# Kernel tuning notes

Hardware: AMD Instinct MI355X
Metric: run time of the kernel (lower is better)

Reference implementation:

```python
import jax, jax.numpy as jnp
import numpy as np

N, L, S, H, D = 2, 4096, 4096, 8, 64


def setup_inputs() -> dict:
    key = jax.random.key(0)
    kq, kk, kv = jax.random.split(key, 3)
    queries = jax.random.normal(kq, (N, L, H, D), dtype=jnp.float32)
    keys = jax.random.normal(kk, (N, S, H, D), dtype=jnp.float32)
    values = jax.random.normal(kv, (N, S, H, D), dtype=jnp.float32)
    return {"queries": queries, "keys": keys, "values": values}


def reference(queries, keys, values):
    # Full (non-fused) scaled dot-product attention, LoFTR FullAttention.
    # QK: [N, L, S, H]
    softmax_temp = 1.0 / jnp.sqrt(jnp.asarray(queries.shape[3], queries.dtype))
    QK = jnp.einsum('nlhd,nshd->nlsh', queries, keys)
    A = jax.nn.softmax(softmax_temp * QK, axis=2)  # softmax over S
    out = jnp.einsum('nlsh,nshd->nlhd', A, values)  # [N, L, H, D]
    return out
```

## Files before the change

kernel.cpp:

```cpp
#include <hip/hip_runtime.h>
#include <hip/hip_bf16.h>

typedef float  f32x4  __attribute__((ext_vector_type(4)));
typedef float  f32x16 __attribute__((ext_vector_type(16)));
typedef short  short8 __attribute__((ext_vector_type(8)));
typedef int    i32x2  __attribute__((ext_vector_type(2)));
typedef unsigned int uint4v __attribute__((ext_vector_type(4)));

#define N_  2
#define L_  4096
#define S_  4096
#define H_  8
#define D_  64
#define HD_ 512
#define KVB 64
#define QB  128
#define NT  (S_ / KVB)

__device__ __forceinline__ unsigned short f2bf(float f) {
  unsigned int u = __builtin_bit_cast(unsigned int, f);
  u += 0x7fffu + ((u >> 16) & 1u);
  return (unsigned short)(u >> 16);
}
__device__ __forceinline__ unsigned short bf16c(float f) {
  return __builtin_bit_cast(unsigned short, __float2bfloat16(f));
}
__device__ __forceinline__ unsigned int pk2(float lo, float hi) {
  unsigned int r;
  asm("v_cvt_pk_bf16_f32 %0, %1, %2" : "=v"(r) : "v"(lo), "v"(hi));
  return r;
}
__device__ __forceinline__ f32x16 zero16() {
  f32x16 v;
  #pragma unroll
  for (int i = 0; i < 16; ++i) v[i] = 0.f;
  return v;
}

#define GLD16(gp, lp)                                                          \
  __builtin_amdgcn_global_load_lds(                                            \
      (const __attribute__((address_space(1))) unsigned int*)(gp),             \
      (__attribute__((address_space(3))) unsigned int*)(lp), 16, 0, 0)

__global__ __launch_bounds__(256, 8)
void prepack(const float* __restrict__ Kg, const float* __restrict__ Vg,
             unsigned short* __restrict__ Kw, unsigned short* __restrict__ Vw) {
  const int b = blockIdx.x;
  const int tid = threadIdx.x;
  const int isV = (b >= 1024);
  const int tb = isV ? b - 1024 : b;
  const int nh = tb >> 6, t = tb & 63;
  const int n = nh >> 3, h = nh & 7;

  if (!isV) {
    const int sl = tid >> 2, d0 = (tid & 3) << 4;
    const float* src = Kg + ((size_t)(n * S_ + t * 64 + sl) * H_ + h) * D_ + d0;
    f32x4 x0 = *(const f32x4*)(src);
    f32x4 x1 = *(const f32x4*)(src + 4);
    f32x4 x2 = *(const f32x4*)(src + 8);
    f32x4 x3 = *(const f32x4*)(src + 12);
    short8 t0, t1;
    t0[0] = (short)f2bf(x0[0]); t0[1] = (short)f2bf(x0[1]);
    t0[2] = (short)f2bf(x0[2]); t0[3] = (short)f2bf(x0[3]);
    t0[4] = (short)f2bf(x1[0]); t0[5] = (short)f2bf(x1[1]);
    t0[6] = (short)f2bf(x1[2]); t0[7] = (short)f2bf(x1[3]);
    t1[0] = (short)f2bf(x2[0]); t1[1] = (short)f2bf(x2[1]);
    t1[2] = (short)f2bf(x2[2]); t1[3] = (short)f2bf(x2[3]);
    t1[4] = (short)f2bf(x3[0]); t1[5] = (short)f2bf(x3[1]);
    t1[6] = (short)f2bf(x3[2]); t1[7] = (short)f2bf(x3[3]);
    unsigned short* dst = Kw + (size_t)tb * 4096 + sl * 64;
    const int b0 = d0 >> 3;
    *(short8*)&dst[((b0)     ^ (sl & 7)) * 8] = t0;
    *(short8*)&dst[((b0 + 1) ^ (sl & 7)) * 8] = t1;
  } else {
    const int d = tid & 63, sb2 = tid >> 6;
    #pragma unroll
    for (int c = 0; c < 2; ++c) {
      const int sblk = sb2 * 2 + c;
      const float* src = Vg + ((size_t)(n * S_ + t * 64 + sblk * 8) * H_ + h) * D_ + d;
      short8 o;
      #pragma unroll
      for (int j = 0; j < 8; ++j) o[j] = (short)f2bf(src[(size_t)j * HD_]);
      *(short8*)&Vw[(size_t)tb * 4096 + sblk * 512 + d * 8] = o;
    }
  }
}

template<int W1, int W2, int DOK, int DOV>
__device__ __forceinline__ void tile_body(
    int t, const int hi, const int c32, const int wv,
    const char* Kt, const char* Vt, const size_t klane, const size_t vlane,
    unsigned short (*Kl)[KVB * D_],
    const short8 qf[4], const short8* vc, short8* vn,
    f32x16& acc0, f32x16& acc1, float& lsum)
{
  const int cur = t & 1;
  asm volatile("s_waitcnt vmcnt(%0)" :: "n"(W1) : "memory");
  __builtin_amdgcn_s_barrier();
  const unsigned short* Kb = Kl[cur];

  short8 kf0[4], kf1[4];
  #pragma unroll
  for (int kc = 0; kc < 4; ++kc) {
    const int ph = (((kc << 1) | hi) ^ (c32 & 7)) * 8;
    kf0[kc] = *(const short8*)&Kb[c32 * 64 + ph];
    kf1[kc] = *(const short8*)&Kb[(32 + c32) * 64 + ph];
  }

  f32x16 s0a = zero16(), s1a = zero16();
  __builtin_amdgcn_s_setprio(1);
  #pragma unroll
  for (int kc = 0; kc < 4; ++kc) {
    s0a = __builtin_amdgcn_mfma_f32_32x32x16_bf16(kf0[kc], qf[kc], s0a, 0, 0, 0);
    s1a = __builtin_amdgcn_mfma_f32_32x32x16_bf16(kf1[kc], qf[kc], s1a, 0, 0, 0);
  }
  __builtin_amdgcn_s_setprio(0);

  asm volatile("s_waitcnt lgkmcnt(0)" ::: "memory");
  __builtin_amdgcn_s_barrier();

  if (DOK) {
    const char* kp = Kt + (size_t)(t + 2) * 8192 + klane;
    GLD16(kp,        &Kl[cur][wv << 9]);
    GLD16(kp + 4096, &Kl[cur][2048 + (wv << 9)]);
  }
  if (DOV) {
    const char* vp = Vt + (size_t)(t + 1) * 8192 + vlane;
    #pragma unroll
    for (int q8 = 0; q8 < 8; ++q8)
      vn[q8] = *(const short8*)(vp + (q8 >> 1) * 2048 + (q8 & 1) * 512);
  }

  #pragma unroll
  for (int r = 0; r < 16; ++r) { s0a[r] = __builtin_amdgcn_exp2f(s0a[r]); lsum += s0a[r]; }
  #pragma unroll
  for (int r = 0; r < 16; ++r) { s1a[r] = __builtin_amdgcn_exp2f(s1a[r]); lsum += s1a[r]; }

  asm volatile("s_waitcnt vmcnt(%0)" :: "n"(W2) : "memory");
  __builtin_amdgcn_sched_barrier(0);

  #pragma unroll
  for (int sc = 0; sc < 4; ++sc) {
    const int c = sc & 1;
    unsigned int c0, c1, c2, c3;
    if (sc < 2) {
      c0 = pk2(s0a[8 * c + 0], s0a[8 * c + 1]);
      c1 = pk2(s0a[8 * c + 2], s0a[8 * c + 3]);
      c2 = pk2(s0a[8 * c + 4], s0a[8 * c + 5]);
      c3 = pk2(s0a[8 * c + 6], s0a[8 * c + 7]);
    } else {
      c0 = pk2(s1a[8 * c + 0], s1a[8 * c + 1]);
      c1 = pk2(s1a[8 * c + 2], s1a[8 * c + 3]);
      c2 = pk2(s1a[8 * c + 4], s1a[8 * c + 5]);
      c3 = pk2(s1a[8 * c + 6], s1a[8 * c + 7]);
    }
    i32x2 r0 = __builtin_amdgcn_permlane32_swap((int)c0, (int)c2, false, false);
    i32x2 r1 = __builtin_amdgcn_permlane32_swap((int)c1, (int)c3, false, false);
    uint4v w = { (unsigned)r0[0], (unsigned)r1[0], (unsigned)r0[1], (unsigned)r1[1] };
    const short8 pa = __builtin_bit_cast(short8, w);
    __builtin_amdgcn_s_setprio(1);
    acc0 = __builtin_amdgcn_mfma_f32_32x32x16_bf16(pa, vc[sc * 2 + 0], acc0, 0, 0, 0);
    acc1 = __builtin_amdgcn_mfma_f32_32x32x16_bf16(pa, vc[sc * 2 + 1], acc1, 0, 0, 0);
    __builtin_amdgcn_s_setprio(0);
  }
}

__global__ __launch_bounds__(256, 2)
void attn_fa4(const float* __restrict__ Qg,
              const unsigned short* __restrict__ Kw,
              const unsigned short* __restrict__ Vw,
              float* __restrict__ Og) {
  __shared__ __align__(16) unsigned short Kl[2][KVB * D_];

  const int tid = threadIdx.x;
  const int wv  = tid >> 6;
  const int ln  = tid & 63;
  const int hi  = ln >> 5;
  const int c32 = ln & 31;

  const int bid = blockIdx.x;
  const int swz = (bid & 7) * 64 + (bid >> 3);
  const int qt  = swz & 31;
  const int nh  = swz >> 5;
  const int h = nh & 7, n = nh >> 3;
  const int qbase = qt * QB;

  const float qs = 0.125f * 1.44269504088896340736f;
  const int qrow = qbase + (wv << 5) + c32;
  const float* qp = Qg + (size_t)(n * L_ + qrow) * HD_ + h * D_ + (hi << 3);
  short8 qf[4];
  #pragma unroll
  for (int kc = 0; kc < 4; ++kc) {
    const float* p = qp + (kc << 4);
    f32x4 a = *(const f32x4*)(p);
    f32x4 b = *(const f32x4*)(p + 4);
    short8 f;
    f[0] = (short)bf16c(a[0] * qs); f[1] = (short)bf16c(a[1] * qs);
    f[2] = (short)bf16c(a[2] * qs); f[3] = (short)bf16c(a[3] * qs);
    f[4] = (short)bf16c(b[0] * qs); f[5] = (short)bf16c(b[1] * qs);
    f[6] = (short)bf16c(b[2] * qs); f[7] = (short)bf16c(b[3] * qs);
    qf[kc] = f;
  }
  asm volatile("s_waitcnt vmcnt(0)" ::: "memory");

  f32x16 acc0 = zero16(), acc1 = zero16();
  float lsum = 0.f;

  const char* Kt = (const char*)(Kw + (size_t)nh * 64 * 4096);
  const char* Vt = (const char*)(Vw + (size_t)nh * 64 * 4096);
  const size_t klane = (size_t)((wv << 10) + (ln << 4));
  const size_t vlane = (size_t)((hi << 10) + (c32 << 4));

  short8 vA[8], vB[8];

  GLD16(Kt + klane,               &Kl[0][wv << 9]);
  GLD16(Kt + klane + 4096,        &Kl[0][2048 + (wv << 9)]);
  GLD16(Kt + 8192 + klane,        &Kl[1][wv << 9]);
  GLD16(Kt + 8192 + klane + 4096, &Kl[1][2048 + (wv << 9)]);
  {
    const char* vp = Vt + vlane;
    #pragma unroll
    for (int q8 = 0; q8 < 8; ++q8)
      vA[q8] = *(const short8*)(vp + (q8 >> 1) * 2048 + (q8 & 1) * 512);
  }

  for (int t = 0; t < NT - 2; t += 2) {
    tile_body<10, 10, 1, 1>(t,     hi, c32, wv, Kt, Vt, klane, vlane, Kl, qf, vA, vB, acc0, acc1, lsum);
    tile_body<10, 10, 1, 1>(t + 1, hi, c32, wv, Kt, Vt, klane, vlane, Kl, qf, vB, vA, acc0, acc1, lsum);
  }
  tile_body<10, 8, 0, 1>(NT - 2, hi, c32, wv, Kt, Vt, klane, vlane, Kl, qf, vA, vB, acc0, acc1, lsum);
  tile_body< 8, 0, 0, 0>(NT - 1, hi, c32, wv, Kt, Vt, klane, vlane, Kl, qf, vB, vA, acc0, acc1, lsum);

  const float full = lsum + __shfl_xor(lsum, 32);
  #pragma unroll
  for (int r = 0; r < 16; ++r) {
    const int qsrc = (r & 3) + 8 * (r >> 2) + 4 * hi;
    const float l = __shfl(full, qsrc);
    const float inv = 1.f / l;
    const int row = qbase + (wv << 5) + qsrc;
    float* op = Og + (size_t)(n * L_ + row) * HD_ + h * D_ + c32;
    op[0]  = acc0[r] * inv;
    op[32] = acc1[r] * inv;
  }
}

extern "C" void kernel_launch(void* const* d_in, const int* in_sizes, int n_in,
                              void* d_out, int out_size, void* d_ws, size_t ws_size,
                              hipStream_t stream) {
  (void)in_sizes; (void)n_in; (void)out_size; (void)ws_size;
  const float* Q = (const float*)d_in[0];
  const float* K = (const float*)d_in[1];
  const float* V = (const float*)d_in[2];
  float* O = (float*)d_out;

  unsigned short* Kw = (unsigned short*)d_ws;
  unsigned short* Vw = Kw + 4194304;
  hipLaunchKernelGGL(prepack, dim3(2048), dim3(256), 0, stream, K, V, Kw, Vw);
  hipLaunchKernelGGL(attn_fa4, dim3(512), dim3(256), 0, stream, Q, Kw, Vw, O);
}
```

Measured before the change: 95.30 us.

## Split KV range across two wave groups per block and combine partial results

Each block now has 8 waves: two groups of four that each process half of the key/value sequence with their own double-buffered LDS K tiles. At the end, the second group writes its partial accumulators and row sums to shared memory, and the first group combines them and writes normalized output. This doubles the number of waves in flight per query tile, which is meant to hide latency better with only 512 blocks. The cost is more LDS, an extra synchronization and a combine step. The row-sum accumulation is also changed to a tree reduction.

```diff
diff --git a/kernel.cpp b/kernel.cpp
--- a/kernel.cpp
+++ b/kernel.cpp
@@ -15,7 +15,7 @@
 #define HD_ 512
 #define KVB 64
 #define QB  128
-#define NT  (S_ / KVB)
+#define NTL 32
 
 __device__ __forceinline__ unsigned short f2bf(float f) {
   unsigned int u = __builtin_bit_cast(unsigned int, f);
@@ -35,6 +35,14 @@
   #pragma unroll
   for (int i = 0; i < 16; ++i) v[i] = 0.f;
   return v;
+}
+__device__ __forceinline__ float tsum16(const f32x16& v) {
+  float a0 = v[0] + v[1],   a1 = v[2] + v[3];
+  float a2 = v[4] + v[5],   a3 = v[6] + v[7];
+  float a4 = v[8] + v[9],   a5 = v[10] + v[11];
+  float a6 = v[12] + v[13], a7 = v[14] + v[15];
+  float b0 = a0 + a1, b1 = a2 + a3, b2 = a4 + a5, b3 = a6 + a7;
+  return (b0 + b1) + (b2 + b3);
 }
 
 #define GLD16(gp, lp)                                                          \
@@ -88,16 +96,16 @@
 
 template<int W1, int W2, int DOK, int DOV>
 __device__ __forceinline__ void tile_body(
-    int t, const int hi, const int c32, const int wv,
-    const char* Kt, const char* Vt, const size_t klane, const size_t vlane,
-    unsigned short (*Kl)[KVB * D_],
+    int t, const int hi, const int c32, const int qw,
+    const char* Kth, const char* Vth, const size_t klane, const size_t vlane,
+    unsigned short (*Klh)[KVB * D_],
     const short8 qf[4], const short8* vc, short8* vn,
     f32x16& acc0, f32x16& acc1, float& lsum)
 {
   const int cur = t & 1;
   asm volatile("s_waitcnt vmcnt(%0)" :: "n"(W1) : "memory");
   __builtin_amdgcn_s_barrier();
-  const unsigned short* Kb = Kl[cur];
+  const unsigned short* Kb = Klh[cur];
 
   short8 kf0[4], kf1[4];
   #pragma unroll
@@ -120,21 +128,22 @@
   __builtin_amdgcn_s_barrier();
 
   if (DOK) {
-    const char* kp = Kt + (size_t)(t + 2) * 8192 + klane;
-    GLD16(kp,        &Kl[cur][wv << 9]);
-    GLD16(kp + 4096, &Kl[cur][2048 + (wv << 9)]);
+    const char* kp = Kth + (size_t)(t + 2) * 8192 + klane;
+    GLD16(kp,        &Klh[cur][qw << 9]);
+    GLD16(kp + 4096, &Klh[cur][2048 + (qw << 9)]);
   }
   if (DOV) {
-    const char* vp = Vt + (size_t)(t + 1) * 8192 + vlane;
+    const char* vp = Vth + (size_t)(t + 1) * 8192 + vlane;
     #pragma unroll
     for (int q8 = 0; q8 < 8; ++q8)
       vn[q8] = *(const short8*)(vp + (q8 >> 1) * 2048 + (q8 & 1) * 512);
   }
 
   #pragma unroll
-  for (int r = 0; r < 16; ++r) { s0a[r] = __builtin_amdgcn_exp2f(s0a[r]); lsum += s0a[r]; }
-  #pragma unroll
-  for (int r = 0; r < 16; ++r) { s1a[r] = __builtin_amdgcn_exp2f(s1a[r]); lsum += s1a[r]; }
+  for (int r = 0; r < 16; ++r) s0a[r] = __builtin_amdgcn_exp2f(s0a[r]);
+  #pragma unroll
+  for (int r = 0; r < 16; ++r) s1a[r] = __builtin_amdgcn_exp2f(s1a[r]);
+  lsum += tsum16(s0a) + tsum16(s1a);
 
   asm volatile("s_waitcnt vmcnt(%0)" :: "n"(W2) : "memory");
   __builtin_amdgcn_sched_barrier(0);
@@ -165,15 +174,18 @@
   }
 }
 
-__global__ __launch_bounds__(256, 2)
-void attn_fa4(const float* __restrict__ Qg,
+__global__ __launch_bounds__(512, 4)
+void attn_fa5(const float* __restrict__ Qg,
               const unsigned short* __restrict__ Kw,
               const unsigned short* __restrict__ Vw,
               float* __restrict__ Og) {
-  __shared__ __align__(16) unsigned short Kl[2][KVB * D_];
+  __shared__ __align__(16) unsigned short Kl[2][2][KVB * D_];
+  __shared__ float CombL[4][32];
 
   const int tid = threadIdx.x;
   const int wv  = tid >> 6;
+  const int qw  = wv & 3;
+  const int sh  = wv >> 2;
   const int ln  = tid & 63;
   const int hi  = ln >> 5;
   const int c32 = ln & 31;
@@ -186,7 +198,7 @@
   const int qbase = qt * QB;
 
   const float qs = 0.125f * 1.44269504088896340736f;
-  const int qrow = qbase + (wv << 5) + c32;
+  const int qrow = qbase + (qw << 5) + c32;
   const float* qp = Qg + (size_t)(n * L_ + qrow) * HD_ + h * D_ + (hi << 3);
   short8 qf[4];
   #pragma unroll
@@ -206,41 +218,57 @@
   f32x16 acc0 = zero16(), acc1 = zero16();
   float lsum = 0.f;
 
-  const char* Kt = (const char*)(Kw + (size_t)nh * 64 * 4096);
-  const char* Vt = (const char*)(Vw + (size_t)nh * 64 * 4096);
-  const size_t klane = (size_t)((wv << 10) + (ln << 4));
+  const char* Kth = (const char*)(Kw + (size_t)nh * 64 * 4096) + (size_t)sh * NTL * 8192;
+  const char* Vth = (const char*)(Vw + (size_t)nh * 64 * 4096) + (size_t)sh * NTL * 8192;
+  const size_t klane = (size_t)((qw << 10) + (ln << 4));
   const size_t vlane = (size_t)((hi << 10) + (c32 << 4));
+  unsigned short (*Klh)[KVB * D_] = Kl[sh];
 
   short8 vA[8], vB[8];
 
-  GLD16(Kt + klane,               &Kl[0][wv << 9]);
-  GLD16(Kt + klane + 4096,        &Kl[0][2048 + (wv << 9)]);
-  GLD16(Kt + 8192 + klane,        &Kl[1][wv << 9]);
-  GLD16(Kt + 8192 + klane + 4096, &Kl[1][2048 + (wv << 9)]);
+  GLD16(Kth + klane,               &Klh[0][qw << 9]);
+  GLD16(Kth + klane + 4096,        &Klh[0][2048 + (qw << 9)]);
+  GLD16(Kth + 8192 + klane,        &Klh[1][qw << 9]);
+  GLD16(Kth + 8192 + klane + 4096, &Klh[1][2048 + (qw << 9)]);
   {
-    const char* vp = Vt + vlane;
+    const char* vp = Vth + vlane;
     #pragma unroll
     for (int q8 = 0; q8 < 8; ++q8)
       vA[q8] = *(const short8*)(vp + (q8 >> 1) * 2048 + (q8 & 1) * 512);
   }
 
-  for (int t = 0; t < NT - 2; t += 2) {
-    tile_body<10, 10, 1, 1>(t,     hi, c32, wv, Kt, Vt, klane, vlane, Kl, qf, vA, vB, acc0, acc1, lsum);
-    tile_body<10, 10, 1, 1>(t + 1, hi, c32, wv, Kt, Vt, klane, vlane, Kl, qf, vB, vA, acc0, acc1, lsum);
-  }
-  tile_body<10, 8, 0, 1>(NT - 2, hi, c32, wv, Kt, Vt, klane, vlane, Kl, qf, vA, vB, acc0, acc1, lsum);
-  tile_body< 8, 0, 0, 0>(NT - 1, hi, c32, wv, Kt, Vt, klane, vlane, Kl, qf, vB, vA, acc0, acc1, lsum);
+  for (int t = 0; t < NTL - 2; t += 2) {
+    tile_body<10, 10, 1, 1>(t,     hi, c32, qw, Kth, Vth, klane, vlane, Klh, qf, vA, vB, acc0, acc1, lsum);
+    tile_body<10, 10, 1, 1>(t + 1, hi, c32, qw, Kth, Vth, klane, vlane, Klh, qf, vB, vA, acc0, acc1, lsum);
+  }
+  tile_body<10, 8, 0, 1>(NTL - 2, hi, c32, qw, Kth, Vth, klane, vlane, Klh, qf, vA, vB, acc0, acc1, lsum);
+  tile_body< 8, 0, 0, 0>(NTL - 1, hi, c32, qw, Kth, Vth, klane, vlane, Klh, qf, vB, vA, acc0, acc1, lsum);
 
   const float full = lsum + __shfl_xor(lsum, 32);
-  #pragma unroll
-  for (int r = 0; r < 16; ++r) {
-    const int qsrc = (r & 3) + 8 * (r >> 2) + 4 * hi;
-    const float l = __shfl(full, qsrc);
-    const float inv = 1.f / l;
-    const int row = qbase + (wv << 5) + qsrc;
-    float* op = Og + (size_t)(n * L_ + row) * HD_ + h * D_ + c32;
-    op[0]  = acc0[r] * inv;
-    op[32] = acc1[r] * inv;
+  float* C = (float*)&Kl[0][0][0] + (size_t)qw * 2048;
+
+  if (sh == 1) {
+    #pragma unroll
+    for (int r = 0; r < 16; ++r) {
+      const int q = (r & 3) + 8 * (r >> 2) + 4 * hi;
+      C[q * 64 + c32]      = acc0[r];
+      C[q * 64 + 32 + c32] = acc1[r];
+    }
+    if (hi == 0) CombL[qw][c32] = full;
+  }
+  __syncthreads();
+  if (sh == 0) {
+    const float ltot = full + CombL[qw][c32];
+    #pragma unroll
+    for (int r = 0; r < 16; ++r) {
+      const int q = (r & 3) + 8 * (r >> 2) + 4 * hi;
+      const float l = __shfl(ltot, q);
+      const float inv = 1.f / l;
+      const int row = qbase + (qw << 5) + q;
+      float* op = Og + (size_t)(n * L_ + row) * HD_ + h * D_ + c32;
+      op[0]  = (acc0[r] + C[q * 64 + c32]) * inv;
+      op[32] = (acc1[r] + C[q * 64 + 32 + c32]) * inv;
+    }
   }
 }
 
@@ -256,5 +284,5 @@
   unsigned short* Kw = (unsigned short*)d_ws;
   unsigned short* Vw = Kw + 4194304;
   hipLaunchKernelGGL(prepack, dim3(2048), dim3(256), 0, stream, K, V, Kw, Vw);
-  hipLaunchKernelGGL(attn_fa4, dim3(512), dim3(256), 0, stream, Q, Kw, Vw, O);
-}
+  hipLaunchKernelGGL(attn_fa5, dim3(512), dim3(512), 0, stream, Q, Kw, Vw, O);
+}
```

New measurement: 309.7 us. 225% more time.
